# Performance work log

Measured on AMD Instinct MI355X. Metric: run time of the kernel, lower is better.

Reference implementation:

```python
import jax, jax.numpy as jnp
import numpy as np
import math

B, N, E, H = 2, 10000, 160000, 128
ET = 8
EPS = 1e-5


def setup_inputs() -> dict:
    key = jax.random.key(0)
    ks = jax.random.split(key, 20)
    s = 1.0 / math.sqrt(H)
    inp = {
        "hidden": jax.random.normal(ks[0], (B, N, H), jnp.float32),
        "time_emb": jax.random.normal(ks[1], (B, N, H), jnp.float32),
        "edge_index": jax.random.randint(ks[2], (2, E), 0, N),
        "edge_type": jax.random.randint(ks[3], (E,), 0, ET),
        # parameters
        "edge_emb": jax.random.normal(ks[4], (ET, H), jnp.float32),
        "Wq": jax.random.normal(ks[5], (H, H), jnp.float32) * s,
        "bq": jnp.zeros((H,), jnp.float32),
        "Wk": jax.random.normal(ks[6], (H, H), jnp.float32) * s,
        "bk": jnp.zeros((H,), jnp.float32),
        "Wv": jax.random.normal(ks[7], (H, H), jnp.float32) * s,
        "bv": jnp.zeros((H,), jnp.float32),
        "We": jax.random.normal(ks[8], (H, 1), jnp.float32) * s,
        "be": jnp.zeros((1,), jnp.float32),
        "W1": jax.random.normal(ks[9], (3 * H, H), jnp.float32) * (1.0 / math.sqrt(3 * H)),
        "b1": jnp.zeros((H,), jnp.float32),
        "W2": jax.random.normal(ks[10], (H, H), jnp.float32) * s,
        "b2": jnp.zeros((H,), jnp.float32),
        "gamma": jnp.ones((H,), jnp.float32),
        "beta": jnp.zeros((H,), jnp.float32),
    }
    return inp


def _forward(hidden, time_emb, edge_index, edge_type, edge_emb,
             Wq, bq, Wk, bk, Wv, bv, We, be, W1, b1, W2, b2, gamma, beta):
    src, tgt = edge_index[0], edge_index[1]
    # edge-wise gathers: [B, E, H]
    src_h = hidden[:, src]
    tgt_h = hidden[:, tgt]
    src_t = time_emb[:, src]
    tgt_t = time_emb[:, tgt]
    edge_h = edge_emb[edge_type][None, :, :]  # [1, E, H] broadcasts over batch

    query = (tgt_h + tgt_t) @ Wq + bq
    key = (src_h + src_t + edge_h) @ Wk + bk
    value = (src_h + edge_h) @ Wv + bv

    logits = jnp.einsum("beh,beh->be", query, key) / math.sqrt(H)
    logits = logits + (edge_h @ We + be)[..., 0]  # edge bias broadcast over batch

    # segment softmax per target node (equivalent to the per-node masked softmax loop)
    lT = logits.T  # [E, B]
    seg_max = jax.ops.segment_max(lT, tgt, num_segments=N)          # [N, B]
    seg_max = jnp.where(jnp.isfinite(seg_max), seg_max, 0.0)
    ex = jnp.exp(lT - seg_max[tgt])                                  # [E, B]
    seg_sum = jax.ops.segment_sum(ex, tgt, num_segments=N)           # [N, B]
    weights = (ex / seg_sum[tgt]).T                                  # [B, E]

    messages = value * weights[..., None]                            # [B, E, H]
    # scatter-add to target nodes
    agg = jax.ops.segment_sum(jnp.swapaxes(messages, 0, 1), tgt, num_segments=N)  # [N, B, H]
    aggregated = jnp.swapaxes(agg, 0, 1)                             # [B, N, H]

    cat = jnp.concatenate([hidden, aggregated, time_emb], axis=-1)   # [B, N, 3H]
    updated = jax.nn.silu(cat @ W1 + b1) @ W2 + b2

    x = hidden + updated  # dropout p=0 -> identity
    mu = jnp.mean(x, axis=-1, keepdims=True)
    var = jnp.var(x, axis=-1, keepdims=True)
    return (x - mu) * jax.lax.rsqrt(var + EPS) * gamma + beta


def reference(hidden, time_emb, edge_index, edge_type, edge_emb,
              Wq, bq, Wk, bk, Wv, bv, We, be, W1, b1, W2, b2, gamma, beta):
    return _forward(hidden, time_emb, edge_index, edge_type, edge_emb,
                    Wq, bq, Wk, bk, Wv, bv, We, be, W1, b1, W2, b2, gamma, beta)
```

## Files before the change

### kernel.cpp

```cpp
#include <hip/hip_runtime.h>
#include <math.h>

constexpr int B_  = 2;
constexpr int N_  = 10000;
constexpr int E_  = 160000;
constexpr int H_  = 128;
constexpr int ET_ = 8;
constexpr float EPS_ = 1e-5f;
constexpr float RSQH = 0.08838834764831845f;

typedef __bf16 bf16x8 __attribute__((ext_vector_type(8)));
typedef short  short8 __attribute__((ext_vector_type(8)));
typedef float  f32x4  __attribute__((ext_vector_type(4)));
typedef unsigned short u16;

__device__ inline u16 bf16b(float f) {
    return __builtin_bit_cast(u16, (__bf16)f);
}

__device__ inline bf16x8 ldfrag(const u16* __restrict__ W, int kc, int nt, int lane) {
    short8 s = *(const short8*)(W + ((kc * 8 + nt) * 64 + lane) * 8);
    return __builtin_bit_cast(bf16x8, s);
}

__global__ __launch_bounds__(256)
void setup_kernel(const float* __restrict__ W1, const float* __restrict__ W2,
                  const float* __restrict__ Wq, const float* __restrict__ Wk,
                  const float* __restrict__ Wv,
                  u16* __restrict__ W1s, u16* __restrict__ W2s,
                  u16* __restrict__ Wqs, u16* __restrict__ Wks, u16* __restrict__ Wvs,
                  const float* __restrict__ edge_emb,
                  const float* __restrict__ bk, const float* __restrict__ bv,
                  const float* __restrict__ We, const float* __restrict__ be,
                  float* __restrict__ Kt, float* __restrict__ Vt, float* __restrict__ eb,
                  const int* __restrict__ tgt, int* __restrict__ hist)
{
    const int bid = blockIdx.x, tid = threadIdx.x;
    if (bid < 56) {
        int unit = bid >> 1, half = bid & 1;
        const float* src; u16* dst; int kc;
        if (unit < 12)      { src = W1; dst = W1s; kc = unit; }
        else if (unit < 16) { src = W2; dst = W2s; kc = unit - 12; }
        else if (unit < 20) { src = Wq; dst = Wqs; kc = unit - 16; }
        else if (unit < 24) { src = Wk; dst = Wks; kc = unit - 20; }
        else                { src = Wv; dst = Wvs; kc = unit - 24; }
        int nt = half * 4 + (tid >> 6), lane = tid & 63;
        int q = lane >> 4, c = lane & 15;
        int kbase = kc * 32 + q * 8;
        int col = nt * 16 + c;
        u16* out = dst + ((kc * 8 + nt) * 64 + lane) * 8;
#pragma unroll
        for (int j = 0; j < 8; ++j)
            out[j] = bf16b(src[(kbase + j) * H_ + col]);
    } else if (bid < 64) {
        int t = bid - 56;
        const float* ep = edge_emb + t * H_;
        __shared__ float red[2];
        int j = tid;
        if (j < 128) {
            float ak = bk[j], av = bv[j];
            for (int d = 0; d < H_; d += 4) {
                float e0 = ep[d], e1 = ep[d+1], e2 = ep[d+2], e3 = ep[d+3];
                ak += e0*Wk[(d+0)*H_+j] + e1*Wk[(d+1)*H_+j] + e2*Wk[(d+2)*H_+j] + e3*Wk[(d+3)*H_+j];
                av += e0*Wv[(d+0)*H_+j] + e1*Wv[(d+1)*H_+j] + e2*Wv[(d+2)*H_+j] + e3*Wv[(d+3)*H_+j];
            }
            Kt[t*H_ + j] = ak;
            Vt[t*H_ + j] = av;
            float pe = ep[j] * We[j];
#pragma unroll
            for (int off = 32; off; off >>= 1) pe += __shfl_xor(pe, off);
            if ((j & 63) == 0) red[j >> 6] = pe;
        }
        __syncthreads();
        if (j == 0) eb[t] = red[0] + red[1] + be[0];
    } else {
        int e = (bid - 64) * 256 + tid;
        if (e < E_) atomicAdd(&hist[tgt[e]], 1);
    }
}

__global__ __launch_bounds__(1024)
void scan_kernel(const int* __restrict__ hist, int* __restrict__ offs,
                 int* __restrict__ cursor)
{
    __shared__ int winc[16];
    const int tid = threadIdx.x, wave = tid >> 6, lane = tid & 63;
    int v[10];
    const int idx0 = tid * 10;
    int tot = 0;
#pragma unroll
    for (int i = 0; i < 10; ++i) {
        int idx = idx0 + i;
        v[i] = (idx < N_) ? hist[idx] : 0;
        tot += v[i];
    }
    int s = tot;
#pragma unroll
    for (int off = 1; off < 64; off <<= 1) {
        int t = __shfl_up(s, off);
        if (lane >= off) s += t;
    }
    if (lane == 63) winc[wave] = s;
    __syncthreads();
    if (tid < 16) {
        int si = winc[tid];
#pragma unroll
        for (int off = 1; off < 16; off <<= 1) {
            int t = __shfl_up(si, off);
            if (tid >= off) si += t;
        }
        winc[tid] = si;
    }
    __syncthreads();
    int wbase = (wave == 0) ? 0 : winc[wave - 1];
    int run = wbase + (s - tot);
#pragma unroll
    for (int i = 0; i < 10; ++i) {
        int idx = idx0 + i;
        if (idx < N_) { offs[idx] = run; cursor[idx] = run; }
        run += v[i];
    }
    if (tid == 0) offs[N_] = winc[15];
}

__global__ __launch_bounds__(256)
void scatter_qkv_kernel(const int* __restrict__ src, const int* __restrict__ tgt,
                        const int* __restrict__ type, int* __restrict__ cursor,
                        int* __restrict__ sorted,
                        const float* __restrict__ hidden, const float* __restrict__ time_emb,
                        const u16* __restrict__ Wqs, const u16* __restrict__ Wks,
                        const u16* __restrict__ Wvs, const float* __restrict__ bq,
                        u16* __restrict__ Q, u16* __restrict__ K, u16* __restrict__ V)
{
    if (blockIdx.x < 625) {
        int e = blockIdx.x * 256 + threadIdx.x;
        if (e < E_) {
            int t = tgt[e];
            int pos = atomicAdd(&cursor[t], 1);
            sorted[pos] = src[e] | (type[e] << 16);
        }
        return;
    }
    const int wv = threadIdx.x >> 6, lane = threadIdx.x & 63;
    const int tile = (blockIdx.x - 625) * 4 + wv;
    if (tile >= (B_ * N_) / 16) return;
    const int nbase = tile * 16;
    const int m = lane & 15, q = lane >> 4;
    const int koff = q * 8;

    bf16x8 aq[4], av[4];
    const float* hp = hidden   + (nbase + m) * H_ + koff;
    const float* tp = time_emb + (nbase + m) * H_ + koff;
#pragma unroll
    for (int kc = 0; kc < 4; ++kc) {
        float4 h0 = *(const float4*)(hp + kc * 32);
        float4 h1 = *(const float4*)(hp + kc * 32 + 4);
        float4 t0 = *(const float4*)(tp + kc * 32);
        float4 t1 = *(const float4*)(tp + kc * 32 + 4);
        bf16x8 fv, fq;
        fv[0]=(__bf16)h0.x; fv[1]=(__bf16)h0.y; fv[2]=(__bf16)h0.z; fv[3]=(__bf16)h0.w;
        fv[4]=(__bf16)h1.x; fv[5]=(__bf16)h1.y; fv[6]=(__bf16)h1.z; fv[7]=(__bf16)h1.w;
        fq[0]=(__bf16)(h0.x+t0.x); fq[1]=(__bf16)(h0.y+t0.y);
        fq[2]=(__bf16)(h0.z+t0.z); fq[3]=(__bf16)(h0.w+t0.w);
        fq[4]=(__bf16)(h1.x+t1.x); fq[5]=(__bf16)(h1.y+t1.y);
        fq[6]=(__bf16)(h1.z+t1.z); fq[7]=(__bf16)(h1.w+t1.w);
        av[kc] = fv; aq[kc] = fq;
    }

    f32x4 accq[8], acck[8], accv[8];
#pragma unroll
    for (int nt = 0; nt < 8; ++nt) { accq[nt] = (f32x4)0.f; acck[nt] = (f32x4)0.f; accv[nt] = (f32x4)0.f; }

#pragma unroll
    for (int kc = 0; kc < 4; ++kc) {
#pragma unroll
        for (int nt = 0; nt < 8; ++nt) {
            bf16x8 bfq = ldfrag(Wqs, kc, nt, lane);
            bf16x8 bfk = ldfrag(Wks, kc, nt, lane);
            bf16x8 bfv = ldfrag(Wvs, kc, nt, lane);
            accq[nt] = __builtin_amdgcn_mfma_f32_16x16x32_bf16(aq[kc], bfq, accq[nt], 0, 0, 0);
            acck[nt] = __builtin_amdgcn_mfma_f32_16x16x32_bf16(aq[kc], bfk, acck[nt], 0, 0, 0);
            accv[nt] = __builtin_amdgcn_mfma_f32_16x16x32_bf16(av[kc], bfv, accv[nt], 0, 0, 0);
        }
    }

#pragma unroll
    for (int nt = 0; nt < 8; ++nt) {
        int col = nt * 16 + m;
        float bqc = bq[col];
#pragma unroll
        for (int r = 0; r < 4; ++r) {
            int node = nbase + q * 4 + r;
            Q[node * H_ + col] = bf16b(accq[nt][r] + bqc);
            K[node * H_ + col] = bf16b(acck[nt][r]);
            V[node * H_ + col] = bf16b(accv[nt][r]);
        }
    }
}

__global__ __launch_bounds__(256)
void attn_mlp_kernel(const u16* __restrict__ Qb, const u16* __restrict__ Kb,
                     const u16* __restrict__ Vb,
                     const float* __restrict__ Kt, const float* __restrict__ Vt,
                     const float* __restrict__ eb,
                     const int* __restrict__ offs, const int* __restrict__ sorted,
                     const float* __restrict__ hidden, const float* __restrict__ time_emb,
                     const u16* __restrict__ W1s, const u16* __restrict__ W2s,
                     const float* __restrict__ b1, const float* __restrict__ b2,
                     const float* __restrict__ gamma, const float* __restrict__ beta,
                     float* __restrict__ out)
{
    __shared__ float bias_s[4][8];
    __shared__ __align__(16) u16 vt_s[8][128];
    __shared__ __align__(16) u16 agg_s[16][136];
    __shared__ __align__(16) u16 h1s[16][136];
    __shared__ float sp[16][4], ssp[16][4];

    const int tid = threadIdx.x;
    const int wv = tid >> 6, lane = tid & 63;
    const int g = lane >> 4, lam = lane & 15;

    for (int idx = tid; idx < ET_ * H_; idx += 256)
        vt_s[idx >> 7][idx & 127] = bf16b(Vt[idx]);
    __syncthreads();

    const int nbase = blockIdx.x * 16;
    const int b = (nbase >= N_) ? 1 : 0;
    const int n0 = nbase - b * N_;
    const u16* __restrict__ Kbb = Kb + (size_t)(b * N_) * H_;
    const u16* __restrict__ Vbb = Vb + (size_t)(b * N_) * H_;

    for (int i = 0; i < 4; ++i) {
        const int nl = wv * 4 + i;
        const int n = n0 + nl;
        const int bn = nbase + nl;
        const int beg = offs[n], end = offs[n + 1];

        float q[8];
        {
            short8 s8 = *(const short8*)(Qb + (size_t)bn * H_ + lam * 8);
            bf16x8 qa = __builtin_bit_cast(bf16x8, s8);
#pragma unroll
            for (int j = 0; j < 8; ++j) q[j] = (float)qa[j];
        }

        {
            const float* k0p = Kt + (2 * g) * H_ + lam * 8;
            const float* k1p = Kt + (2 * g + 1) * H_ + lam * 8;
            float p0 = 0.f, p1 = 0.f;
#pragma unroll
            for (int j = 0; j < 8; ++j) { p0 += q[j] * k0p[j]; p1 += q[j] * k1p[j]; }
#pragma unroll
            for (int msk = 1; msk < 16; msk <<= 1) {
                p0 += __shfl_xor(p0, msk);
                p1 += __shfl_xor(p1, msk);
            }
            if (lam == 0) {
                bias_s[wv][2 * g]     = p0 * RSQH + eb[2 * g];
                bias_s[wv][2 * g + 1] = p1 * RSQH + eb[2 * g + 1];
            }
        }

        float m_g = -INFINITY, l_g = 0.f;
        float acc[8];
#pragma unroll
        for (int j = 0; j < 8; ++j) acc[j] = 0.f;

        int c = beg + g;
        for (; c + 4 < end; c += 8) {
            int pk0 = sorted[c];
            int pk1 = sorted[c + 4];
            int s0 = pk0 & 0xFFFF, t0 = pk0 >> 16;
            int s1 = pk1 & 0xFFFF, t1 = pk1 >> 16;
            short8 k80 = *(const short8*)(Kbb + (size_t)s0 * H_ + lam * 8);
            short8 k81 = *(const short8*)(Kbb + (size_t)s1 * H_ + lam * 8);
            short8 v80 = *(const short8*)(Vbb + (size_t)s0 * H_ + lam * 8);
            short8 v81 = *(const short8*)(Vbb + (size_t)s1 * H_ + lam * 8);
            short8 vt80 = *(const short8*)(&vt_s[t0][lam * 8]);
            short8 vt81 = *(const short8*)(&vt_s[t1][lam * 8]);
            bf16x8 ka0 = __builtin_bit_cast(bf16x8, k80);
            bf16x8 ka1 = __builtin_bit_cast(bf16x8, k81);
            float p0 = 0.f, p1 = 0.f;
#pragma unroll
            for (int j = 0; j < 8; ++j) {
                p0 += q[j] * (float)ka0[j];
                p1 += q[j] * (float)ka1[j];
            }
#pragma unroll
            for (int msk = 1; msk < 16; msk <<= 1) {
                p0 += __shfl_xor(p0, msk);
                p1 += __shfl_xor(p1, msk);
            }
            float lg0 = p0 * RSQH + bias_s[wv][t0];
            float lg1 = p1 * RSQH + bias_s[wv][t1];
            float mx = fmaxf(lg0, lg1);
            if (mx > m_g + 8.f) {
                float rs = __expf(m_g - mx);
                l_g *= rs;
#pragma unroll
                for (int j = 0; j < 8; ++j) acc[j] *= rs;
                m_g = mx;
            }
            float w0 = __expf(lg0 - m_g);
            float w1 = __expf(lg1 - m_g);
            l_g += w0 + w1;
            bf16x8 va0  = __builtin_bit_cast(bf16x8, v80);
            bf16x8 va1  = __builtin_bit_cast(bf16x8, v81);
            bf16x8 vta0 = __builtin_bit_cast(bf16x8, vt80);
            bf16x8 vta1 = __builtin_bit_cast(bf16x8, vt81);
#pragma unroll
            for (int j = 0; j < 8; ++j)
                acc[j] += w0 * ((float)va0[j] + (float)vta0[j])
                        + w1 * ((float)va1[j] + (float)vta1[j]);
        }
        if (c < end) {
            int pk0 = sorted[c];
            int s0 = pk0 & 0xFFFF, t0 = pk0 >> 16;
            short8 k80 = *(const short8*)(Kbb + (size_t)s0 * H_ + lam * 8);
            short8 v80 = *(const short8*)(Vbb + (size_t)s0 * H_ + lam * 8);
            short8 vt80 = *(const short8*)(&vt_s[t0][lam * 8]);
            bf16x8 ka0 = __builtin_bit_cast(bf16x8, k80);
            float p0 = 0.f;
#pragma unroll
            for (int j = 0; j < 8; ++j) p0 += q[j] * (float)ka0[j];
#pragma unroll
            for (int msk = 1; msk < 16; msk <<= 1) p0 += __shfl_xor(p0, msk);
            float lg0 = p0 * RSQH + bias_s[wv][t0];
            if (lg0 > m_g + 8.f) {
                float rs = __expf(m_g - lg0);
                l_g *= rs;
#pragma unroll
                for (int j = 0; j < 8; ++j) acc[j] *= rs;
                m_g = lg0;
            }
            float w0 = __expf(lg0 - m_g);
            l_g += w0;
            bf16x8 va0  = __builtin_bit_cast(bf16x8, v80);
            bf16x8 vta0 = __builtin_bit_cast(bf16x8, vt80);
#pragma unroll
            for (int j = 0; j < 8; ++j)
                acc[j] += w0 * ((float)va0[j] + (float)vta0[j]);
        }

        float M = fmaxf(m_g, __shfl_xor(m_g, 16));
        M = fmaxf(M, __shfl_xor(M, 32));
        float rs = (m_g == M) ? 1.f : __expf(m_g - M);
        l_g *= rs;
#pragma unroll
        for (int j = 0; j < 8; ++j) {
            acc[j] *= rs;
            acc[j] += __shfl_xor(acc[j], 16);
            acc[j] += __shfl_xor(acc[j], 32);
        }
        l_g += __shfl_xor(l_g, 16);
        l_g += __shfl_xor(l_g, 32);

        if (g == 0) {
            float invL = (end > beg) ? 1.f / l_g : 0.f;
            bf16x8 o;
#pragma unroll
            for (int j = 0; j < 8; ++j) o[j] = (__bf16)(acc[j] * invL);
            *(short8*)(&agg_s[nl][lam * 8]) = __builtin_bit_cast(short8, o);
        }
    }
    __syncthreads();

    const int m = lane & 15, q = lane >> 4;
    const int koff = q * 8;

    bf16x8 a[12];
    const float* hp = hidden   + (size_t)(nbase + m) * H_ + koff;
    const float* tp = time_emb + (size_t)(nbase + m) * H_ + koff;
#pragma unroll
    for (int kc = 0; kc < 4; ++kc) {
        float4 h0 = *(const float4*)(hp + kc * 32);
        float4 h1 = *(const float4*)(hp + kc * 32 + 4);
        float4 t0 = *(const float4*)(tp + kc * 32);
        float4 t1 = *(const float4*)(tp + kc * 32 + 4);
        bf16x8 fh, ft;
        fh[0]=(__bf16)h0.x; fh[1]=(__bf16)h0.y; fh[2]=(__bf16)h0.z; fh[3]=(__bf16)h0.w;
        fh[4]=(__bf16)h1.x; fh[5]=(__bf16)h1.y; fh[6]=(__bf16)h1.z; fh[7]=(__bf16)h1.w;
        ft[0]=(__bf16)t0.x; ft[1]=(__bf16)t0.y; ft[2]=(__bf16)t0.z; ft[3]=(__bf16)t0.w;
        ft[4]=(__bf16)t1.x; ft[5]=(__bf16)t1.y; ft[6]=(__bf16)t1.z; ft[7]=(__bf16)t1.w;
        a[0 * 4 + kc] = fh;
        a[2 * 4 + kc] = ft;
        short8 s8 = *(const short8*)(&agg_s[m][kc * 32 + koff]);
        a[1 * 4 + kc] = __builtin_bit_cast(bf16x8, s8);
    }

    f32x4 acc1[2];
    acc1[0] = (f32x4)0.f; acc1[1] = (f32x4)0.f;
#pragma unroll
    for (int kc = 0; kc < 12; ++kc) {
#pragma unroll
        for (int ntl = 0; ntl < 2; ++ntl) {
            bf16x8 bf = ldfrag(W1s, kc, 2 * wv + ntl, lane);
            acc1[ntl] = __builtin_amdgcn_mfma_f32_16x16x32_bf16(a[kc], bf, acc1[ntl], 0, 0, 0);
        }
    }
#pragma unroll
    for (int ntl = 0; ntl < 2; ++ntl) {
        int col = (2 * wv + ntl) * 16 + m;
        float bb = b1[col];
#pragma unroll
        for (int r = 0; r < 4; ++r) {
            float v = acc1[ntl][r] + bb;
            float h = v / (1.f + __expf(-v));
            h1s[q * 4 + r][col] = bf16b(h);
        }
    }
    __syncthreads();

    f32x4 acc2[2];
    acc2[0] = (f32x4)0.f; acc2[1] = (f32x4)0.f;
#pragma unroll
    for (int kc = 0; kc < 4; ++kc) {
        short8 s8 = *(const short8*)(&h1s[m][kc * 32 + koff]);
        bf16x8 a2 = __builtin_bit_cast(bf16x8, s8);
#pragma unroll
        for (int ntl = 0; ntl < 2; ++ntl) {
            bf16x8 bf = ldfrag(W2s, kc, 2 * wv + ntl, lane);
            acc2[ntl] = __builtin_amdgcn_mfma_f32_16x16x32_bf16(a2, bf, acc2[ntl], 0, 0, 0);
        }
    }

    float x[2][4];
#pragma unroll
    for (int ntl = 0; ntl < 2; ++ntl) {
        int col = (2 * wv + ntl) * 16 + m;
        float bb = b2[col];
#pragma unroll
        for (int r = 0; r < 4; ++r) {
            int node = nbase + q * 4 + r;
            x[ntl][r] = hidden[(size_t)node * H_ + col] + acc2[ntl][r] + bb;
        }
    }
#pragma unroll
    for (int r = 0; r < 4; ++r) {
        float s  = x[0][r] + x[1][r];
        float ss = x[0][r] * x[0][r] + x[1][r] * x[1][r];
#pragma unroll
        for (int off = 1; off < 16; off <<= 1) {
            s  += __shfl_xor(s, off);
            ss += __shfl_xor(ss, off);
        }
        if (m == 0) { sp[q * 4 + r][wv] = s; ssp[q * 4 + r][wv] = ss; }
    }
    __syncthreads();
#pragma unroll
    for (int r = 0; r < 4; ++r) {
        int nl = q * 4 + r;
        float s  = sp[nl][0]  + sp[nl][1]  + sp[nl][2]  + sp[nl][3];
        float ss = ssp[nl][0] + ssp[nl][1] + ssp[nl][2] + ssp[nl][3];
        float mu  = s * (1.f / H_);
        float var = ss * (1.f / H_) - mu * mu;
        float rsn = rsqrtf(var + EPS_);
        int node = nbase + nl;
#pragma unroll
        for (int ntl = 0; ntl < 2; ++ntl) {
            int col = (2 * wv + ntl) * 16 + m;
            out[(size_t)node * H_ + col] = (x[ntl][r] - mu) * rsn * gamma[col] + beta[col];
        }
    }
}

extern "C" void kernel_launch(void* const* d_in, const int* in_sizes, int n_in,
                              void* d_out, int out_size, void* d_ws, size_t ws_size,
                              hipStream_t stream)
{
    const float* hidden   = (const float*)d_in[0];
    const float* time_emb = (const float*)d_in[1];
    const int*   eidx     = (const int*)d_in[2];
    const int*   etype    = (const int*)d_in[3];
    const float* edge_emb = (const float*)d_in[4];
    const float* Wq = (const float*)d_in[5];
    const float* bq = (const float*)d_in[6];
    const float* Wk = (const float*)d_in[7];
    const float* bk = (const float*)d_in[8];
    const float* Wv = (const float*)d_in[9];
    const float* bv = (const float*)d_in[10];
    const float* We = (const float*)d_in[11];
    const float* be = (const float*)d_in[12];
    const float* W1 = (const float*)d_in[13];
    const float* b1 = (const float*)d_in[14];
    const float* W2 = (const float*)d_in[15];
    const float* b2 = (const float*)d_in[16];
    const float* gamma = (const float*)d_in[17];
    const float* beta  = (const float*)d_in[18];
    float* out = (float*)d_out;

    constexpr int BNH = B_ * N_ * H_;
    u16* Qb   = (u16*)d_ws;
    u16* Kb   = Qb + BNH;
    u16* Vb   = Kb + BNH;
    float* Kt  = (float*)(Vb + BNH);
    float* Vt  = Kt + ET_ * H_;
    float* ebt = Vt + ET_ * H_;
    int* hist   = (int*)(ebt + ET_);
    int* offs   = hist + N_;
    int* cursor = offs + (N_ + 1);
    int* sorted = cursor + N_;
    uintptr_t wp = (uintptr_t)(sorted + E_);
    wp = (wp + 15) & ~(uintptr_t)15;
    u16* W1s = (u16*)wp;
    u16* W2s = W1s + 384 * 128;
    u16* Wqs = W2s + 128 * 128;
    u16* Wks = Wqs + 128 * 128;
    u16* Wvs = Wks + 128 * 128;

    const int* esrc = eidx;
    const int* etgt = eidx + E_;

    hipMemsetAsync(hist, 0, N_ * sizeof(int), stream);

    setup_kernel<<<64 + (E_ + 255) / 256, 256, 0, stream>>>(
        W1, W2, Wq, Wk, Wv, W1s, W2s, Wqs, Wks, Wvs,
        edge_emb, bk, bv, We, be, Kt, Vt, ebt, etgt, hist);
    scan_kernel<<<1, 1024, 0, stream>>>(hist, offs, cursor);
    scatter_qkv_kernel<<<625 + 313, 256, 0, stream>>>(
        esrc, etgt, etype, cursor, sorted,
        hidden, time_emb, Wqs, Wks, Wvs, bq, Qb, Kb, Vb);
    attn_mlp_kernel<<<(B_ * N_) / 16, 256, 0, stream>>>(
        Qb, Kb, Vb, Kt, Vt, ebt, offs, sorted,
        hidden, time_emb, W1s, W2s, b1, b2, gamma, beta, out);
}
```

Measured before the change: 205.7 us.

## Use 16 waves per block: one wave per node in attention, 8 waves for MLP

The attention/MLP kernel now launches 1024 threads per block so each of the 16 waves handles one target node's attention instead of each of 4 waves looping over 4 nodes. The MLP and LayerNorm stages run on only 8 of the 16 waves, each computing one 16-column tile instead of two, and the LayerNorm partial sums grow to 8 slots. The aim is more parallelism and latency hiding in the gather-heavy attention phase. The cost is 8 idle waves during the MLP, larger blocks that may cap occupancy under the 1024-thread launch bound, and extra barrier cost.

```diff
diff --git a/kernel.cpp b/kernel.cpp
--- a/kernel.cpp
+++ b/kernel.cpp
@@ -198,7 +198,7 @@
     }
 }
 
-__global__ __launch_bounds__(256)
+__global__ __launch_bounds__(1024)
 void attn_mlp_kernel(const u16* __restrict__ Qb, const u16* __restrict__ Kb,
                      const u16* __restrict__ Vb,
                      const float* __restrict__ Kt, const float* __restrict__ Vt,
@@ -210,18 +210,18 @@
                      const float* __restrict__ gamma, const float* __restrict__ beta,
                      float* __restrict__ out)
 {
-    __shared__ float bias_s[4][8];
+    __shared__ float bias_s[16][8];
     __shared__ __align__(16) u16 vt_s[8][128];
     __shared__ __align__(16) u16 agg_s[16][136];
     __shared__ __align__(16) u16 h1s[16][136];
-    __shared__ float sp[16][4], ssp[16][4];
+    __shared__ float sp[16][8], ssp[16][8];
 
     const int tid = threadIdx.x;
     const int wv = tid >> 6, lane = tid & 63;
     const int g = lane >> 4, lam = lane & 15;
 
-    for (int idx = tid; idx < ET_ * H_; idx += 256)
-        vt_s[idx >> 7][idx & 127] = bf16b(Vt[idx]);
+    if (tid < ET_ * H_)
+        vt_s[tid >> 7][tid & 127] = bf16b(Vt[tid]);
     __syncthreads();
 
     const int nbase = blockIdx.x * 16;
@@ -230,8 +230,8 @@
     const u16* __restrict__ Kbb = Kb + (size_t)(b * N_) * H_;
     const u16* __restrict__ Vbb = Vb + (size_t)(b * N_) * H_;
 
-    for (int i = 0; i < 4; ++i) {
-        const int nl = wv * 4 + i;
+    {
+        const int nl = wv;
         const int n = n0 + nl;
         const int bn = nbase + nl;
         const int beg = offs[n], end = offs[n + 1];
@@ -367,99 +367,92 @@
 
     const int m = lane & 15, q = lane >> 4;
     const int koff = q * 8;
-
-    bf16x8 a[12];
-    const float* hp = hidden   + (size_t)(nbase + m) * H_ + koff;
-    const float* tp = time_emb + (size_t)(nbase + m) * H_ + koff;
-#pragma unroll
-    for (int kc = 0; kc < 4; ++kc) {
-        float4 h0 = *(const float4*)(hp + kc * 32);
-        float4 h1 = *(const float4*)(hp + kc * 32 + 4);
-        float4 t0 = *(const float4*)(tp + kc * 32);
-        float4 t1 = *(const float4*)(tp + kc * 32 + 4);
-        bf16x8 fh, ft;
-        fh[0]=(__bf16)h0.x; fh[1]=(__bf16)h0.y; fh[2]=(__bf16)h0.z; fh[3]=(__bf16)h0.w;
-        fh[4]=(__bf16)h1.x; fh[5]=(__bf16)h1.y; fh[6]=(__bf16)h1.z; fh[7]=(__bf16)h1.w;
-        ft[0]=(__bf16)t0.x; ft[1]=(__bf16)t0.y; ft[2]=(__bf16)t0.z; ft[3]=(__bf16)t0.w;
-        ft[4]=(__bf16)t1.x; ft[5]=(__bf16)t1.y; ft[6]=(__bf16)t1.z; ft[7]=(__bf16)t1.w;
-        a[0 * 4 + kc] = fh;
-        a[2 * 4 + kc] = ft;
-        short8 s8 = *(const short8*)(&agg_s[m][kc * 32 + koff]);
-        a[1 * 4 + kc] = __builtin_bit_cast(bf16x8, s8);
-    }
-
-    f32x4 acc1[2];
-    acc1[0] = (f32x4)0.f; acc1[1] = (f32x4)0.f;
-#pragma unroll
-    for (int kc = 0; kc < 12; ++kc) {
-#pragma unroll
-        for (int ntl = 0; ntl < 2; ++ntl) {
-            bf16x8 bf = ldfrag(W1s, kc, 2 * wv + ntl, lane);
-            acc1[ntl] = __builtin_amdgcn_mfma_f32_16x16x32_bf16(a[kc], bf, acc1[ntl], 0, 0, 0);
-        }
-    }
-#pragma unroll
-    for (int ntl = 0; ntl < 2; ++ntl) {
-        int col = (2 * wv + ntl) * 16 + m;
+    float x[4];
+    f32x4 acc2;
+
+    if (wv < 8) {
+        bf16x8 a[12];
+        const float* hp = hidden   + (size_t)(nbase + m) * H_ + koff;
+        const float* tp = time_emb + (size_t)(nbase + m) * H_ + koff;
+#pragma unroll
+        for (int kc = 0; kc < 4; ++kc) {
+            float4 h0 = *(const float4*)(hp + kc * 32);
+            float4 h1 = *(const float4*)(hp + kc * 32 + 4);
+            float4 t0 = *(const float4*)(tp + kc * 32);
+            float4 t1 = *(const float4*)(tp + kc * 32 + 4);
+            bf16x8 fh, ft;
+            fh[0]=(__bf16)h0.x; fh[1]=(__bf16)h0.y; fh[2]=(__bf16)h0.z; fh[3]=(__bf16)h0.w;
+            fh[4]=(__bf16)h1.x; fh[5]=(__bf16)h1.y; fh[6]=(__bf16)h1.z; fh[7]=(__bf16)h1.w;
+            ft[0]=(__bf16)t0.x; ft[1]=(__bf16)t0.y; ft[2]=(__bf16)t0.z; ft[3]=(__bf16)t0.w;
+            ft[4]=(__bf16)t1.x; ft[5]=(__bf16)t1.y; ft[6]=(__bf16)t1.z; ft[7]=(__bf16)t1.w;
+            a[0 * 4 + kc] = fh;
+            a[2 * 4 + kc] = ft;
+            short8 s8 = *(const short8*)(&agg_s[m][kc * 32 + koff]);
+            a[1 * 4 + kc] = __builtin_bit_cast(bf16x8, s8);
+        }
+
+        f32x4 acc1 = (f32x4)0.f;
+#pragma unroll
+        for (int kc = 0; kc < 12; ++kc) {
+            bf16x8 bf = ldfrag(W1s, kc, wv, lane);
+            acc1 = __builtin_amdgcn_mfma_f32_16x16x32_bf16(a[kc], bf, acc1, 0, 0, 0);
+        }
+        int col = wv * 16 + m;
         float bb = b1[col];
 #pragma unroll
         for (int r = 0; r < 4; ++r) {
-            float v = acc1[ntl][r] + bb;
+            float v = acc1[r] + bb;
             float h = v / (1.f + __expf(-v));
             h1s[q * 4 + r][col] = bf16b(h);
         }
     }
     __syncthreads();
 
-    f32x4 acc2[2];
-    acc2[0] = (f32x4)0.f; acc2[1] = (f32x4)0.f;
-#pragma unroll
-    for (int kc = 0; kc < 4; ++kc) {
-        short8 s8 = *(const short8*)(&h1s[m][kc * 32 + koff]);
-        bf16x8 a2 = __builtin_bit_cast(bf16x8, s8);
-#pragma unroll
-        for (int ntl = 0; ntl < 2; ++ntl) {
-            bf16x8 bf = ldfrag(W2s, kc, 2 * wv + ntl, lane);
-            acc2[ntl] = __builtin_amdgcn_mfma_f32_16x16x32_bf16(a2, bf, acc2[ntl], 0, 0, 0);
-        }
-    }
-
-    float x[2][4];
-#pragma unroll
-    for (int ntl = 0; ntl < 2; ++ntl) {
-        int col = (2 * wv + ntl) * 16 + m;
+    if (wv < 8) {
+        acc2 = (f32x4)0.f;
+#pragma unroll
+        for (int kc = 0; kc < 4; ++kc) {
+            short8 s8 = *(const short8*)(&h1s[m][kc * 32 + koff]);
+            bf16x8 a2 = __builtin_bit_cast(bf16x8, s8);
+            bf16x8 bf = ldfrag(W2s, kc, wv, lane);
+            acc2 = __builtin_amdgcn_mfma_f32_16x16x32_bf16(a2, bf, acc2, 0, 0, 0);
+        }
+
+        int col = wv * 16 + m;
         float bb = b2[col];
 #pragma unroll
         for (int r = 0; r < 4; ++r) {
             int node = nbase + q * 4 + r;
-            x[ntl][r] = hidden[(size_t)node * H_ + col] + acc2[ntl][r] + bb;
-        }
-    }
-#pragma unroll
-    for (int r = 0; r < 4; ++r) {
-        float s  = x[0][r] + x[1][r];
-        float ss = x[0][r] * x[0][r] + x[1][r] * x[1][r];
-#pragma unroll
-        for (int off = 1; off < 16; off <<= 1) {
-            s  += __shfl_xor(s, off);
-            ss += __shfl_xor(ss, off);
-        }
-        if (m == 0) { sp[q * 4 + r][wv] = s; ssp[q * 4 + r][wv] = ss; }
+            x[r] = hidden[(size_t)node * H_ + col] + acc2[r] + bb;
+        }
+#pragma unroll
+        for (int r = 0; r < 4; ++r) {
+            float s  = x[r];
+            float ss = x[r] * x[r];
+#pragma unroll
+            for (int off = 1; off < 16; off <<= 1) {
+                s  += __shfl_xor(s, off);
+                ss += __shfl_xor(ss, off);
+            }
+            if (m == 0) { sp[q * 4 + r][wv] = s; ssp[q * 4 + r][wv] = ss; }
+        }
     }
     __syncthreads();
-#pragma unroll
-    for (int r = 0; r < 4; ++r) {
-        int nl = q * 4 + r;
-        float s  = sp[nl][0]  + sp[nl][1]  + sp[nl][2]  + sp[nl][3];
-        float ss = ssp[nl][0] + ssp[nl][1] + ssp[nl][2] + ssp[nl][3];
-        float mu  = s * (1.f / H_);
-        float var = ss * (1.f / H_) - mu * mu;
-        float rsn = rsqrtf(var + EPS_);
-        int node = nbase + nl;
-#pragma unroll
-        for (int ntl = 0; ntl < 2; ++ntl) {
-            int col = (2 * wv + ntl) * 16 + m;
-            out[(size_t)node * H_ + col] = (x[ntl][r] - mu) * rsn * gamma[col] + beta[col];
+
+    if (wv < 8) {
+        int col = wv * 16 + m;
+#pragma unroll
+        for (int r = 0; r < 4; ++r) {
+            int nl = q * 4 + r;
+            float s  = (sp[nl][0]  + sp[nl][1])  + (sp[nl][2]  + sp[nl][3])
+                     + (sp[nl][4]  + sp[nl][5])  + (sp[nl][6]  + sp[nl][7]);
+            float ss = (ssp[nl][0] + ssp[nl][1]) + (ssp[nl][2] + ssp[nl][3])
+                     + (ssp[nl][4] + ssp[nl][5]) + (ssp[nl][6] + ssp[nl][7]);
+            float mu  = s * (1.f / H_);
+            float var = ss * (1.f / H_) - mu * mu;
+            float rsn = rsqrtf(var + EPS_);
+            int node = nbase + nl;
+            out[(size_t)node * H_ + col] = (x[r] - mu) * rsn * gamma[col] + beta[col];
         }
     }
 }
@@ -520,7 +513,7 @@
     scatter_qkv_kernel<<<625 + 313, 256, 0, stream>>>(
         esrc, etgt, etype, cursor, sorted,
         hidden, time_emb, Wqs, Wks, Wvs, bq, Qb, Kb, Vb);
-    attn_mlp_kernel<<<(B_ * N_) / 16, 256, 0, stream>>>(
+    attn_mlp_kernel<<<(B_ * N_) / 16, 1024, 0, stream>>>(
         Qb, Kb, Vb, Kt, Vt, ebt, offs, sorted,
         hidden, time_emb, W1s, W2s, b1, b2, gamma, beta, out);
 }
```

Result: slower. 211.4 us (+2.8%).
